# Optimization experiments

Measured on AMD Instinct MI355X. Metric: run time of the kernel, lower is better.

Reference implementation:

```python
import jax, jax.numpy as jnp
import numpy as np

H = 51      # hidden_size
IN = 1      # input_size
T = 512     # timesteps
B = 1024    # batch


def setup_inputs() -> dict:
    key = jax.random.key(0)
    ks = jax.random.split(key, 11)
    s = 1.0 / np.sqrt(H)  # PyTorch default init scale for LSTMCell/Linear
    u = lambda k, shape: jax.random.uniform(k, shape, jnp.float32, -s, s)
    return {
        "input": jax.random.normal(ks[0], (T, B, IN), jnp.float32),
        "W_ih1": u(ks[1], (4 * H, IN)),
        "W_hh1": u(ks[2], (4 * H, H)),
        "b_ih1": u(ks[3], (4 * H,)),
        "b_hh1": u(ks[4], (4 * H,)),
        "W_ih2": u(ks[5], (4 * H, H)),
        "W_hh2": u(ks[6], (4 * H, H)),
        "b_ih2": u(ks[7], (4 * H,)),
        "b_hh2": u(ks[8], (4 * H,)),
        "W_lin": u(ks[9], (1, H)),
        "b_lin": u(ks[10], (1,)),
        "future": 0,
    }


def _cell(x, h, c, W_ih, W_hh, b_ih, b_hh):
    # PyTorch LSTMCell: gates ordered (i, f, g, o)
    gates = x @ W_ih.T + h @ W_hh.T + (b_ih + b_hh)  # (B, 4H)
    i, f, g, o = jnp.split(gates, 4, axis=-1)
    c_new = jax.nn.sigmoid(f) * c + jax.nn.sigmoid(i) * jnp.tanh(g)
    h_new = jax.nn.sigmoid(o) * jnp.tanh(c_new)
    return h_new, c_new


def reference(input, W_ih1, W_hh1, b_ih1, b_hh1,
              W_ih2, W_hh2, b_ih2, b_hh2, W_lin, b_lin, future):
    n = input.shape[1]
    z = jnp.zeros((n, H), input.dtype)

    def step(carry, x_t):
        h1, c1, h2, c2 = carry
        h1, c1 = _cell(x_t, h1, c1, W_ih1, W_hh1, b_ih1, b_hh1)
        h2, c2 = _cell(h1, h2, c2, W_ih2, W_hh2, b_ih2, b_hh2)
        out = h2 @ W_lin.T + b_lin  # (B, 1)
        return (h1, c1, h2, c2), out

    carry, outs = jax.lax.scan(step, (z, z, z, z), input)  # outs: (T, B, 1)

    if future > 0:  # static Python int -> static branch
        def fstep(carry, _):
            h1, c1, h2, c2, out = carry
            h1, c1 = _cell(out, h1, c1, W_ih1, W_hh1, b_ih1, b_hh1)
            h2, c2 = _cell(h1, h2, c2, W_ih2, W_hh2, b_ih2, b_hh2)
            out = h2 @ W_lin.T + b_lin
            return (h1, c1, h2, c2, out), out

        h1, c1, h2, c2 = carry
        _, fouts = jax.lax.scan(fstep, (h1, c1, h2, c2, outs[-1]), None,
                                length=future)
        outs = jnp.concatenate([outs, fouts], axis=0)

    # torch cat(dim=1) of (B,1) slices -> (B, T+future)
    return outs[..., 0].T
```

## Files before the change

kernel.cpp:

```cpp
#include <hip/hip_runtime.h>


#define Hs    51
#define Ts    512
#define Bs    1024
#define NB    16
#define NT    512
#define SA    136
#define XCOL  51
#define H2COL 64

typedef __attribute__((ext_vector_type(8))) short bf16x8;
typedef __attribute__((ext_vector_type(4))) float f32x4;
typedef __attribute__((ext_vector_type(4))) int   i32x4;
typedef unsigned short u16;

__device__ __forceinline__ float sig_(float x)  { return 1.0f / (1.0f + __expf(-x)); }
__device__ __forceinline__ float tanh_(float x) { float e = __expf(2.0f * x); return 1.0f - 2.0f / (e + 1.0f); }
__device__ __forceinline__ u16 bfh_(float x) {
    unsigned u = __float_as_uint(x);
    return (u16)((u + 0x7FFFu + ((u >> 16) & 1u)) >> 16);
}
__device__ __forceinline__ float bff_(u16 h) { return __uint_as_float(((unsigned)h) << 16); }

struct FragHL { bf16x8 h; bf16x8 l; };

__device__ __forceinline__ FragHL mkB1(const float* __restrict__ Whh1,
                                       const float* __restrict__ Wih1,
                                       int row, bool rv, int ks, int ch) {
    bf16x8 h = {0,0,0,0,0,0,0,0}, l = {0,0,0,0,0,0,0,0};
    #pragma unroll
    for (int j = 0; j < 8; ++j) {
        const int k = ks * 32 + ch * 8 + j;
        float v = 0.f;
        if (rv) {
            if (k < Hs)         v = Whh1[row * Hs + k];
            else if (k == XCOL) v = Wih1[row];
        }
        u16 hh = bfh_(v);
        h[j] = (short)hh;
        l[j] = (short)bfh_(v - bff_(hh));
    }
    FragHL r; r.h = h; r.l = l; return r;
}

__device__ __forceinline__ FragHL mkB2(const float* __restrict__ Wih2,
                                       const float* __restrict__ Whh2,
                                       int row, bool rv, int ks, int ch) {
    bf16x8 h = {0,0,0,0,0,0,0,0}, l = {0,0,0,0,0,0,0,0};
    #pragma unroll
    for (int j = 0; j < 8; ++j) {
        const int k = ks * 32 + ch * 8 + j;
        float v = 0.f;
        if (rv) {
            if (k < Hs)                              v = Wih2[row * Hs + k];
            else if (k >= H2COL && k < H2COL + Hs)   v = Whh2[row * Hs + (k - H2COL)];
        }
        u16 hh = bfh_(v);
        h[j] = (short)hh;
        l[j] = (short)bfh_(v - bff_(hh));
    }
    FragHL r; r.h = h; r.l = l; return r;
}

__device__ __align__(16) u16   g_pack[NT * 32 * 8];
__device__ __align__(16) float g_bias[NT * 4];

__global__ __launch_bounds__(NT) void prep_kernel(
    const float* __restrict__ W_ih1, const float* __restrict__ W_hh1,
    const float* __restrict__ b_ih1, const float* __restrict__ b_hh1,
    const float* __restrict__ W_ih2, const float* __restrict__ W_hh2,
    const float* __restrict__ b_ih2, const float* __restrict__ b_hh2)
{
    const int tid  = threadIdx.x;
    const int lane = tid & 63;
    const int wv   = tid >> 6;
    const int role = wv >> 2;
    const int jg   = wv & 3;
    const int m    = lane & 15;
    const int ch   = lane >> 4;
    const int jrow = jg * 16 + m;
    const bool rv  = jrow < Hs;
    const int nks  = role ? 4 : 2;
    u16* base = &g_pack[tid * 256];

    for (int g = 0; g < 4; ++g) {
        const int row = g * Hs + jrow;
        g_bias[tid * 4 + g] = rv ? (role ? (b_ih2[row] + b_hh2[row])
                                         : (b_ih1[row] + b_hh1[row]))
                                 : 0.f;
        for (int s = 0; s < nks; ++s) {
            FragHL f = role ? mkB2(W_ih2, W_hh2, row, rv, s, ch)
                            : mkB1(W_hh1, W_ih1, row, rv, s, ch);
            *(bf16x8*)(base + (g * (2 * nks) + 2 * s + 0) * 8) = f.h;
            *(bf16x8*)(base + (g * (2 * nks) + 2 * s + 1) * 8) = f.l;
        }
    }
}

__device__ __forceinline__ bf16x8 ldfrag(const u16* p) {
    i32x4 v = *(const i32x4*)p;
    asm volatile("" : "+v"(v));
    union { i32x4 i; bf16x8 b; } u;
    u.i = v;
    return u.b;
}

#define MF(ACC, AFH, AFL, BH, BL)                                              \
    ACC = __builtin_amdgcn_mfma_f32_16x16x32_bf16(AFH, BL, ACC, 0, 0, 0);      \
    ACC = __builtin_amdgcn_mfma_f32_16x16x32_bf16(AFL, BH, ACC, 0, 0, 0);      \
    ACC = __builtin_amdgcn_mfma_f32_16x16x32_bf16(AFH, BH, ACC, 0, 0, 0);

__global__ __launch_bounds__(NT)
__attribute__((amdgpu_waves_per_eu(2, 2)))
void lstm2_kernel(
    const float* __restrict__ x,
    const float* __restrict__ W_lin,
    const float* __restrict__ b_lin,
    float* __restrict__ out)
{
    __shared__ __align__(16) u16   Ah[2][NB * SA];
    __shared__ __align__(16) u16   Al[2][NB * SA];
    __shared__ __align__(16) float xs[Ts][NB];
    __shared__ __align__(16) float h2f[2][NB][68];
    __shared__ __align__(16) float wlin_s[64];
    __shared__ float blin_sh;

    const int tid  = threadIdx.x;
    const int lane = tid & 63;
    const int wv   = tid >> 6;
    const int role = wv >> 2;
    const int jg   = wv & 3;
    const int m    = lane & 15;
    const int ch   = lane >> 4;
    const int bg0  = blockIdx.x * NB;
    const int  jrow = jg * 16 + m;
    const bool rv   = jrow < Hs;

    for (int i = tid; i < Ts * NB; i += NT) {
        int t = i >> 4, b = i & 15;
        xs[t][b] = x[t * Bs + bg0 + b];
    }
    for (int i = tid; i < 2 * NB * SA; i += NT) {
        ((u16*)Ah)[i] = 0;
        ((u16*)Al)[i] = 0;
    }
    for (int i = tid; i < 2 * NB * 68; i += NT) ((float*)h2f)[i] = 0.f;
    if (tid < 64) wlin_s[tid] = (tid < Hs) ? W_lin[tid] : 0.f;
    if (tid == 0) blin_sh = b_lin[0];
    __syncthreads();

    if (tid < NB) {
        float xv = x[bg0 + tid];
        u16 hh = bfh_(xv);
        Ah[1][tid * SA + XCOL] = hh;
        Al[1][tid * SA + XCOL] = bfh_(xv - bff_(hh));
    }

    f32x4 bb4 = *(const f32x4*)&g_bias[tid * 4];
    asm volatile("" : "+v"(bb4));
    const float bbI = bb4.x, bbF = bb4.y, bbG = bb4.z, bbO = bb4.w;

    const u16* pk = &g_pack[tid * 256];

    float cc0 = 0.f, cc1 = 0.f, cc2 = 0.f, cc3 = 0.f;
    __syncthreads();

    if (role == 0) {
        bf16x8 bI0h = ldfrag(pk + (0*4 + 0)*8), bI0l = ldfrag(pk + (0*4 + 1)*8);
        bf16x8 bI1h = ldfrag(pk + (0*4 + 2)*8), bI1l = ldfrag(pk + (0*4 + 3)*8);
        bf16x8 bF0h = ldfrag(pk + (1*4 + 0)*8), bF0l = ldfrag(pk + (1*4 + 1)*8);
        bf16x8 bF1h = ldfrag(pk + (1*4 + 2)*8), bF1l = ldfrag(pk + (1*4 + 3)*8);
        bf16x8 bG0h = ldfrag(pk + (2*4 + 0)*8), bG0l = ldfrag(pk + (2*4 + 1)*8);
        bf16x8 bG1h = ldfrag(pk + (2*4 + 2)*8), bG1l = ldfrag(pk + (2*4 + 3)*8);
        bf16x8 bO0h = ldfrag(pk + (3*4 + 0)*8), bO0l = ldfrag(pk + (3*4 + 1)*8);
        bf16x8 bO1h = ldfrag(pk + (3*4 + 2)*8), bO1l = ldfrag(pk + (3*4 + 3)*8);

        for (int it = 0; it <= Ts + 1; ++it) {
            const int pR = (it - 1) & 1;
            const int pW = it & 1;
            if (it < Ts) {
                const u16* ph = &Ah[pR][m * SA + ch * 8];
                const u16* pl = &Al[pR][m * SA + ch * 8];
                bf16x8 A0h = *(const bf16x8*)(ph);
                bf16x8 A0l = *(const bf16x8*)(pl);
                bf16x8 A1h = *(const bf16x8*)(ph + 32);
                bf16x8 A1l = *(const bf16x8*)(pl + 32);
                f32x4 aI = {bbI, bbI, bbI, bbI};
                f32x4 aF = {bbF, bbF, bbF, bbF};
                f32x4 aG = {bbG, bbG, bbG, bbG};
                f32x4 aO = {bbO, bbO, bbO, bbO};
                MF(aI, A0h, A0l, bI0h, bI0l)  MF(aF, A0h, A0l, bF0h, bF0l)
                MF(aG, A0h, A0l, bG0h, bG0l)  MF(aO, A0h, A0l, bO0h, bO0l)
                MF(aI, A1h, A1l, bI1h, bI1l)  MF(aF, A1h, A1l, bF1h, bF1l)
                MF(aG, A1h, A1l, bG1h, bG1l)  MF(aO, A1h, A1l, bO1h, bO1l)
                #define E1STEP(RR, CC)                                         \
                {                                                              \
                    float iv = sig_ (aI[RR]);                                  \
                    float fv = sig_ (aF[RR]);                                  \
                    float gv = tanh_(aG[RR]);                                  \
                    float ov = sig_ (aO[RR]);                                  \
                    CC = fmaf(fv, CC, iv * gv);                                \
                    float hv = ov * tanh_(CC);                                 \
                    if (rv) {                                                  \
                        const int b = 4 * ch + RR;                             \
                        u16 hh = bfh_(hv);                                     \
                        Ah[pW][b * SA + jrow] = hh;                            \
                        Al[pW][b * SA + jrow] = bfh_(hv - bff_(hh));           \
                    }                                                          \
                }
                E1STEP(0, cc0) E1STEP(1, cc1) E1STEP(2, cc2) E1STEP(3, cc3)
                #undef E1STEP
            }
            if (jg == 0 && lane < NB && (it + 1) < Ts) {
                float xv = xs[it + 1][lane];
                u16 hh = bfh_(xv);
                Ah[pW][lane * SA + XCOL] = hh;
                Al[pW][lane * SA + XCOL] = bfh_(xv - bff_(hh));
            }
            if (it >= 2) {
                const float* hp = &h2f[it & 1][4 * jg + ch][0];
                float s = wlin_s[m]      * hp[m]
                        + wlin_s[m + 16] * hp[m + 16]
                        + wlin_s[m + 32] * hp[m + 32]
                        + wlin_s[m + 48] * hp[m + 48];
                s += __shfl_xor(s, 1);
                s += __shfl_xor(s, 2);
                s += __shfl_xor(s, 4);
                s += __shfl_xor(s, 8);
                if (m == 0) out[(bg0 + 4 * jg + ch) * Ts + (it - 2)] = s + blin_sh;
            }
            __syncthreads();
        }
    } else {
        bf16x8 cI0h = ldfrag(pk + (0*8 + 0)*8), cI0l = ldfrag(pk + (0*8 + 1)*8);
        bf16x8 cI1h = ldfrag(pk + (0*8 + 2)*8), cI1l = ldfrag(pk + (0*8 + 3)*8);
        bf16x8 cI2h = ldfrag(pk + (0*8 + 4)*8), cI2l = ldfrag(pk + (0*8 + 5)*8);
        bf16x8 cI3h = ldfrag(pk + (0*8 + 6)*8), cI3l = ldfrag(pk + (0*8 + 7)*8);
        bf16x8 cF0h = ldfrag(pk + (1*8 + 0)*8), cF0l = ldfrag(pk + (1*8 + 1)*8);
        bf16x8 cF1h = ldfrag(pk + (1*8 + 2)*8), cF1l = ldfrag(pk + (1*8 + 3)*8);
        bf16x8 cF2h = ldfrag(pk + (1*8 + 4)*8), cF2l = ldfrag(pk + (1*8 + 5)*8);
        bf16x8 cF3h = ldfrag(pk + (1*8 + 6)*8), cF3l = ldfrag(pk + (1*8 + 7)*8);
        bf16x8 cG0h = ldfrag(pk + (2*8 + 0)*8), cG0l = ldfrag(pk + (2*8 + 1)*8);
        bf16x8 cG1h = ldfrag(pk + (2*8 + 2)*8), cG1l = ldfrag(pk + (2*8 + 3)*8);
        bf16x8 cG2h = ldfrag(pk + (2*8 + 4)*8), cG2l = ldfrag(pk + (2*8 + 5)*8);
        bf16x8 cG3h = ldfrag(pk + (2*8 + 6)*8), cG3l = ldfrag(pk + (2*8 + 7)*8);
        bf16x8 cO0h = ldfrag(pk + (3*8 + 0)*8), cO0l = ldfrag(pk + (3*8 + 1)*8);
        bf16x8 cO1h = ldfrag(pk + (3*8 + 2)*8), cO1l = ldfrag(pk + (3*8 + 3)*8);
        bf16x8 cO2h = ldfrag(pk + (3*8 + 4)*8), cO2l = ldfrag(pk + (3*8 + 5)*8);
        bf16x8 cO3h = ldfrag(pk + (3*8 + 6)*8), cO3l = ldfrag(pk + (3*8 + 7)*8);

        for (int it = 0; it <= Ts + 1; ++it) {
            const int pR = (it - 1) & 1;
            const int pW = it & 1;
            if (it >= 1 && it <= Ts) {
                const u16* ph = &Ah[pR][m * SA + ch * 8];
                const u16* pl = &Al[pR][m * SA + ch * 8];
                bf16x8 A0h = *(const bf16x8*)(ph);
                bf16x8 A0l = *(const bf16x8*)(pl);
                bf16x8 A1h = *(const bf16x8*)(ph + 32);
                bf16x8 A1l = *(const bf16x8*)(pl + 32);
                bf16x8 A2h = *(const bf16x8*)(ph + 64);
                bf16x8 A2l = *(const bf16x8*)(pl + 64);
                bf16x8 A3h = *(const bf16x8*)(ph + 96);
                bf16x8 A3l = *(const bf16x8*)(pl + 96);
                f32x4 aI = {bbI, bbI, bbI, bbI};
                f32x4 aF = {bbF, bbF, bbF, bbF};
                f32x4 aG = {bbG, bbG, bbG, bbG};
                f32x4 aO = {bbO, bbO, bbO, bbO};
                MF(aI, A0h, A0l, cI0h, cI0l)  MF(aF, A0h, A0l, cF0h, cF0l)
                MF(aG, A0h, A0l, cG0h, cG0l)  MF(aO, A0h, A0l, cO0h, cO0l)
                MF(aI, A1h, A1l, cI1h, cI1l)  MF(aF, A1h, A1l, cF1h, cF1l)
                MF(aG, A1h, A1l, cG1h, cG1l)  MF(aO, A1h, A1l, cO1h, cO1l)
                MF(aI, A2h, A2l, cI2h, cI2l)  MF(aF, A2h, A2l, cF2h, cF2l)
                MF(aG, A2h, A2l, cG2h, cG2l)  MF(aO, A2h, A2l, cO2h, cO2l)
                MF(aI, A3h, A3l, cI3h, cI3l)  MF(aF, A3h, A3l, cF3h, cF3l)
                MF(aG, A3h, A3l, cG3h, cG3l)  MF(aO, A3h, A3l, cO3h, cO3l)
                const int pE = (it - 1) & 1;
                #define E2STEP(RR, CC)                                         \
                {                                                              \
                    float iv = sig_ (aI[RR]);                                  \
                    float fv = sig_ (aF[RR]);                                  \
                    float gv = tanh_(aG[RR]);                                  \
                    float ov = sig_ (aO[RR]);                                  \
                    CC = fmaf(fv, CC, iv * gv);                                \
                    float hv = ov * tanh_(CC);                                 \
                    if (rv) {                                                  \
                        const int b = 4 * ch + RR;                             \
                        u16 hh = bfh_(hv);                                     \
                        Ah[pW][b * SA + H2COL + jrow] = hh;                    \
                        Al[pW][b * SA + H2COL + jrow] = bfh_(hv - bff_(hh));   \
                        h2f[pE][b][jrow] = hv;                                 \
                    }                                                          \
                }
                E2STEP(0, cc0) E2STEP(1, cc1) E2STEP(2, cc2) E2STEP(3, cc3)
                #undef E2STEP
            }
            __syncthreads();
        }
    }
}

extern "C" void kernel_launch(void* const* d_in, const int* in_sizes, int n_in,
                              void* d_out, int out_size, void* d_ws, size_t ws_size,
                              hipStream_t stream) {
    const float* x     = (const float*)d_in[0];
    const float* W_ih1 = (const float*)d_in[1];
    const float* W_hh1 = (const float*)d_in[2];
    const float* b_ih1 = (const float*)d_in[3];
    const float* b_hh1 = (const float*)d_in[4];
    const float* W_ih2 = (const float*)d_in[5];
    const float* W_hh2 = (const float*)d_in[6];
    const float* b_ih2 = (const float*)d_in[7];
    const float* b_hh2 = (const float*)d_in[8];
    const float* W_lin = (const float*)d_in[9];
    const float* b_lin = (const float*)d_in[10];
    float* out = (float*)d_out;

    prep_kernel<<<1, NT, 0, stream>>>(W_ih1, W_hh1, b_ih1, b_hh1,
                                      W_ih2, W_hh2, b_ih2, b_hh2);
    lstm2_kernel<<<Bs / NB, NT, 0, stream>>>(x, W_lin, b_lin, out);
}
```

Baseline: 1.052 ms.

## Split MFMA accumulation chains, precompute split-bf16 inputs, buffer outputs in LDS

Each gate's hi/lo bf16 MFMA products now go into independent accumulator chains that are summed at the end, replacing one long dependent chain, to cut MFMA latency on the recurrent critical path. Input x is split into hi/lo bf16 once during preload rather than every step. Linear-layer outputs are collected in a shared-memory buffer and written to global memory coalesced after the loop, instead of as strided per-step stores. The waves_per_eu attribute is dropped and W_lin is hoisted into registers, which may raise register pressure and change occupancy; the extra 32KB of LDS also counts against the shared-memory budget.

```diff
diff --git a/kernel.cpp b/kernel.cpp
--- a/kernel.cpp
+++ b/kernel.cpp
@@ -106,24 +106,21 @@
     return u.b;
 }
 
-#define MF(ACC, AFH, AFL, BH, BL)                                              \
-    ACC = __builtin_amdgcn_mfma_f32_16x16x32_bf16(AFH, BL, ACC, 0, 0, 0);      \
-    ACC = __builtin_amdgcn_mfma_f32_16x16x32_bf16(AFL, BH, ACC, 0, 0, 0);      \
-    ACC = __builtin_amdgcn_mfma_f32_16x16x32_bf16(AFH, BH, ACC, 0, 0, 0);
+#define MFMA_(A, B, C) __builtin_amdgcn_mfma_f32_16x16x32_bf16(A, B, C, 0, 0, 0)
 
 __global__ __launch_bounds__(NT)
-__attribute__((amdgpu_waves_per_eu(2, 2)))
 void lstm2_kernel(
     const float* __restrict__ x,
     const float* __restrict__ W_lin,
     const float* __restrict__ b_lin,
     float* __restrict__ out)
 {
-    __shared__ __align__(16) u16   Ah[2][NB * SA];
-    __shared__ __align__(16) u16   Al[2][NB * SA];
-    __shared__ __align__(16) float xs[Ts][NB];
-    __shared__ __align__(16) float h2f[2][NB][68];
-    __shared__ __align__(16) float wlin_s[64];
+    __shared__ __align__(16) u16      Ah[2][NB * SA];
+    __shared__ __align__(16) u16      Al[2][NB * SA];
+    __shared__ __align__(16) unsigned xs32[Ts][NB];
+    __shared__ __align__(16) float    h2f[2][NB][68];
+    __shared__ __align__(16) float    ybuf[NB][Ts];
+    __shared__ __align__(16) float    wlin_s[64];
     __shared__ float blin_sh;
 
     const int tid  = threadIdx.x;
@@ -139,7 +136,10 @@
 
     for (int i = tid; i < Ts * NB; i += NT) {
         int t = i >> 4, b = i & 15;
-        xs[t][b] = x[t * Bs + bg0 + b];
+        float xv = x[t * Bs + bg0 + b];
+        u16 hh = bfh_(xv);
+        u16 hl = bfh_(xv - bff_(hh));
+        xs32[t][b] = (unsigned)hh | ((unsigned)hl << 16);
     }
     for (int i = tid; i < 2 * NB * SA; i += NT) {
         ((u16*)Ah)[i] = 0;
@@ -151,10 +151,9 @@
     __syncthreads();
 
     if (tid < NB) {
-        float xv = x[bg0 + tid];
-        u16 hh = bfh_(xv);
-        Ah[1][tid * SA + XCOL] = hh;
-        Al[1][tid * SA + XCOL] = bfh_(xv - bff_(hh));
+        unsigned v = xs32[0][tid];
+        Ah[1][tid * SA + XCOL] = (u16)v;
+        Al[1][tid * SA + XCOL] = (u16)(v >> 16);
     }
 
     f32x4 bb4 = *(const f32x4*)&g_bias[tid * 4];
@@ -165,6 +164,10 @@
 
     float cc0 = 0.f, cc1 = 0.f, cc2 = 0.f, cc3 = 0.f;
     __syncthreads();
+
+    const float wl0 = wlin_s[m],      wl1 = wlin_s[m + 16];
+    const float wl2 = wlin_s[m + 32], wl3 = wlin_s[m + 48];
+    const float blin_r = blin_sh;
 
     if (role == 0) {
         bf16x8 bI0h = ldfrag(pk + (0*4 + 0)*8), bI0l = ldfrag(pk + (0*4 + 1)*8);
@@ -186,14 +189,22 @@
                 bf16x8 A0l = *(const bf16x8*)(pl);
                 bf16x8 A1h = *(const bf16x8*)(ph + 32);
                 bf16x8 A1l = *(const bf16x8*)(pl + 32);
-                f32x4 aI = {bbI, bbI, bbI, bbI};
-                f32x4 aF = {bbF, bbF, bbF, bbF};
-                f32x4 aG = {bbG, bbG, bbG, bbG};
-                f32x4 aO = {bbO, bbO, bbO, bbO};
-                MF(aI, A0h, A0l, bI0h, bI0l)  MF(aF, A0h, A0l, bF0h, bF0l)
-                MF(aG, A0h, A0l, bG0h, bG0l)  MF(aO, A0h, A0l, bO0h, bO0l)
-                MF(aI, A1h, A1l, bI1h, bI1l)  MF(aF, A1h, A1l, bF1h, bF1l)
-                MF(aG, A1h, A1l, bG1h, bG1l)  MF(aO, A1h, A1l, bO1h, bO1l)
+                #define L1GATE(OUT, BB, B0h, B0l, B1h, B1l)                    \
+                {                                                              \
+                    f32x4 p = {BB, BB, BB, BB};                                \
+                    f32x4 q = {0.f, 0.f, 0.f, 0.f};                            \
+                    f32x4 r = {0.f, 0.f, 0.f, 0.f};                            \
+                    p = MFMA_(A0h, B0h, p); p = MFMA_(A1h, B1h, p);            \
+                    q = MFMA_(A0l, B0h, q); q = MFMA_(A1l, B1h, q);            \
+                    r = MFMA_(A0h, B0l, r); r = MFMA_(A1h, B1l, r);            \
+                    OUT = (p + q) + r;                                         \
+                }
+                f32x4 aI, aF, aG, aO;
+                L1GATE(aI, bbI, bI0h, bI0l, bI1h, bI1l)
+                L1GATE(aF, bbF, bF0h, bF0l, bF1h, bF1l)
+                L1GATE(aG, bbG, bG0h, bG0l, bG1h, bG1l)
+                L1GATE(aO, bbO, bO0h, bO0l, bO1h, bO1l)
+                #undef L1GATE
                 #define E1STEP(RR, CC)                                         \
                 {                                                              \
                     float iv = sig_ (aI[RR]);                                  \
@@ -213,22 +224,19 @@
                 #undef E1STEP
             }
             if (jg == 0 && lane < NB && (it + 1) < Ts) {
-                float xv = xs[it + 1][lane];
-                u16 hh = bfh_(xv);
-                Ah[pW][lane * SA + XCOL] = hh;
-                Al[pW][lane * SA + XCOL] = bfh_(xv - bff_(hh));
+                unsigned v = xs32[it + 1][lane];
+                Ah[pW][lane * SA + XCOL] = (u16)v;
+                Al[pW][lane * SA + XCOL] = (u16)(v >> 16);
             }
             if (it >= 2) {
                 const float* hp = &h2f[it & 1][4 * jg + ch][0];
-                float s = wlin_s[m]      * hp[m]
-                        + wlin_s[m + 16] * hp[m + 16]
-                        + wlin_s[m + 32] * hp[m + 32]
-                        + wlin_s[m + 48] * hp[m + 48];
+                float s = wl0 * hp[m] + wl1 * hp[m + 16]
+                        + wl2 * hp[m + 32] + wl3 * hp[m + 48];
                 s += __shfl_xor(s, 1);
                 s += __shfl_xor(s, 2);
                 s += __shfl_xor(s, 4);
                 s += __shfl_xor(s, 8);
-                if (m == 0) out[(bg0 + 4 * jg + ch) * Ts + (it - 2)] = s + blin_sh;
+                if (m == 0) ybuf[4 * jg + ch][it - 2] = s + blin_r;
             }
             __syncthreads();
         }
@@ -264,18 +272,24 @@
                 bf16x8 A2l = *(const bf16x8*)(pl + 64);
                 bf16x8 A3h = *(const bf16x8*)(ph + 96);
                 bf16x8 A3l = *(const bf16x8*)(pl + 96);
-                f32x4 aI = {bbI, bbI, bbI, bbI};
-                f32x4 aF = {bbF, bbF, bbF, bbF};
-                f32x4 aG = {bbG, bbG, bbG, bbG};
-                f32x4 aO = {bbO, bbO, bbO, bbO};
-                MF(aI, A0h, A0l, cI0h, cI0l)  MF(aF, A0h, A0l, cF0h, cF0l)
-                MF(aG, A0h, A0l, cG0h, cG0l)  MF(aO, A0h, A0l, cO0h, cO0l)
-                MF(aI, A1h, A1l, cI1h, cI1l)  MF(aF, A1h, A1l, cF1h, cF1l)
-                MF(aG, A1h, A1l, cG1h, cG1l)  MF(aO, A1h, A1l, cO1h, cO1l)
-                MF(aI, A2h, A2l, cI2h, cI2l)  MF(aF, A2h, A2l, cF2h, cF2l)
-                MF(aG, A2h, A2l, cG2h, cG2l)  MF(aO, A2h, A2l, cO2h, cO2l)
-                MF(aI, A3h, A3l, cI3h, cI3l)  MF(aF, A3h, A3l, cF3h, cF3l)
-                MF(aG, A3h, A3l, cG3h, cG3l)  MF(aO, A3h, A3l, cO3h, cO3l)
+                #define L2GATE(OUT, BB, C0h, C0l, C1h, C1l, C2h, C2l, C3h, C3l)\
+                {                                                              \
+                    f32x4 p = {BB, BB, BB, BB};                                \
+                    f32x4 r = {0.f, 0.f, 0.f, 0.f};                            \
+                    p = MFMA_(A0h, C0h, p); p = MFMA_(A1h, C1h, p);            \
+                    p = MFMA_(A2h, C2h, p); p = MFMA_(A3h, C3h, p);            \
+                    p = MFMA_(A0l, C0h, p); p = MFMA_(A1l, C1h, p);            \
+                    p = MFMA_(A2l, C2h, p); p = MFMA_(A3l, C3h, p);            \
+                    r = MFMA_(A0h, C0l, r); r = MFMA_(A1h, C1l, r);            \
+                    r = MFMA_(A2h, C2l, r); r = MFMA_(A3h, C3l, r);            \
+                    OUT = p + r;                                               \
+                }
+                f32x4 aI, aF, aG, aO;
+                L2GATE(aI, bbI, cI0h, cI0l, cI1h, cI1l, cI2h, cI2l, cI3h, cI3l)
+                L2GATE(aF, bbF, cF0h, cF0l, cF1h, cF1l, cF2h, cF2l, cF3h, cF3l)
+                L2GATE(aG, bbG, cG0h, cG0l, cG1h, cG1l, cG2h, cG2l, cG3h, cG3l)
+                L2GATE(aO, bbO, cO0h, cO0l, cO1h, cO1l, cO2h, cO2l, cO3h, cO3l)
+                #undef L2GATE
                 const int pE = (it - 1) & 1;
                 #define E2STEP(RR, CC)                                         \
                 {                                                              \
@@ -299,6 +313,12 @@
             __syncthreads();
         }
     }
+
+    __syncthreads();
+    for (int i = tid; i < NB * Ts; i += NT) {
+        int b = i >> 9, t = i & (Ts - 1);
+        out[(bg0 + b) * Ts + t] = ybuf[b][t];
+    }
 }
 
 extern "C" void kernel_launch(void* const* d_in, const int* in_sizes, int n_in,
```

After: 1.114 ms. +5.9%, slower.

## Merge layer-1 and layer-2 wave roles into single 256-thread block per batch tile

Applied to the files above, without the earlier changes.

Instead of 8 waves split into layer-1 and layer-2 roles, each of 4 waves now computes both LSTM layers sequentially within a timestep, holding both weight sets in registers. Block size halves and waves-per-EU is set to 1, cutting barrier participants and letting each wave run more work per barrier. The input is also pre-split into bf16 hi/lo pairs once at load time, and the linear-head weights are hoisted into registers. The cost is serialising the two layers' MFMA chains within a wave (less parallelism per step) and much higher register pressure.

```diff
diff --git a/kernel.cpp b/kernel.cpp
--- a/kernel.cpp
+++ b/kernel.cpp
@@ -5,7 +5,7 @@
 #define Ts    512
 #define Bs    1024
 #define NB    16
-#define NT    512
+#define NT    256
 #define SA    136
 #define XCOL  51
 #define H2COL 64
@@ -63,8 +63,8 @@
     FragHL r; r.h = h; r.l = l; return r;
 }
 
-__device__ __align__(16) u16   g_pack[NT * 32 * 8];
-__device__ __align__(16) float g_bias[NT * 4];
+__device__ __align__(16) u16   g_pack[NT * 48 * 8];
+__device__ __align__(16) float g_bias[NT * 8];
 
 __global__ __launch_bounds__(NT) void prep_kernel(
     const float* __restrict__ W_ih1, const float* __restrict__ W_hh1,
@@ -74,26 +74,26 @@
 {
     const int tid  = threadIdx.x;
     const int lane = tid & 63;
-    const int wv   = tid >> 6;
-    const int role = wv >> 2;
-    const int jg   = wv & 3;
+    const int jg   = tid >> 6;
     const int m    = lane & 15;
     const int ch   = lane >> 4;
     const int jrow = jg * 16 + m;
     const bool rv  = jrow < Hs;
-    const int nks  = role ? 4 : 2;
-    u16* base = &g_pack[tid * 256];
+    u16* base = &g_pack[tid * 384];
 
     for (int g = 0; g < 4; ++g) {
         const int row = g * Hs + jrow;
-        g_bias[tid * 4 + g] = rv ? (role ? (b_ih2[row] + b_hh2[row])
-                                         : (b_ih1[row] + b_hh1[row]))
-                                 : 0.f;
-        for (int s = 0; s < nks; ++s) {
-            FragHL f = role ? mkB2(W_ih2, W_hh2, row, rv, s, ch)
-                            : mkB1(W_hh1, W_ih1, row, rv, s, ch);
-            *(bf16x8*)(base + (g * (2 * nks) + 2 * s + 0) * 8) = f.h;
-            *(bf16x8*)(base + (g * (2 * nks) + 2 * s + 1) * 8) = f.l;
+        g_bias[tid * 8 + g]     = rv ? (b_ih1[row] + b_hh1[row]) : 0.f;
+        g_bias[tid * 8 + 4 + g] = rv ? (b_ih2[row] + b_hh2[row]) : 0.f;
+        for (int s = 0; s < 2; ++s) {
+            FragHL f = mkB1(W_hh1, W_ih1, row, rv, s, ch);
+            *(bf16x8*)(base + (g * 4 + s * 2 + 0) * 8) = f.h;
+            *(bf16x8*)(base + (g * 4 + s * 2 + 1) * 8) = f.l;
+        }
+        for (int s = 0; s < 4; ++s) {
+            FragHL f = mkB2(W_ih2, W_hh2, row, rv, s, ch);
+            *(bf16x8*)(base + (16 + g * 8 + s * 2 + 0) * 8) = f.h;
+            *(bf16x8*)(base + (16 + g * 8 + s * 2 + 1) * 8) = f.l;
         }
     }
 }
@@ -106,31 +106,30 @@
     return u.b;
 }
 
+#define MFMA_(A, B, C) __builtin_amdgcn_mfma_f32_16x16x32_bf16(A, B, C, 0, 0, 0)
 #define MF(ACC, AFH, AFL, BH, BL)                                              \
-    ACC = __builtin_amdgcn_mfma_f32_16x16x32_bf16(AFH, BL, ACC, 0, 0, 0);      \
-    ACC = __builtin_amdgcn_mfma_f32_16x16x32_bf16(AFL, BH, ACC, 0, 0, 0);      \
-    ACC = __builtin_amdgcn_mfma_f32_16x16x32_bf16(AFH, BH, ACC, 0, 0, 0);
+    ACC = MFMA_(AFH, BL, ACC);                                                 \
+    ACC = MFMA_(AFL, BH, ACC);                                                 \
+    ACC = MFMA_(AFH, BH, ACC);
 
 __global__ __launch_bounds__(NT)
-__attribute__((amdgpu_waves_per_eu(2, 2)))
+__attribute__((amdgpu_waves_per_eu(1, 1)))
 void lstm2_kernel(
     const float* __restrict__ x,
     const float* __restrict__ W_lin,
     const float* __restrict__ b_lin,
     float* __restrict__ out)
 {
-    __shared__ __align__(16) u16   Ah[2][NB * SA];
-    __shared__ __align__(16) u16   Al[2][NB * SA];
-    __shared__ __align__(16) float xs[Ts][NB];
-    __shared__ __align__(16) float h2f[2][NB][68];
-    __shared__ __align__(16) float wlin_s[64];
+    __shared__ __align__(16) u16      Ah[2][NB * SA];
+    __shared__ __align__(16) u16      Al[2][NB * SA];
+    __shared__ __align__(16) unsigned xs32[Ts][NB];
+    __shared__ __align__(16) float    h2f[2][NB][68];
+    __shared__ __align__(16) float    wlin_s[64];
     __shared__ float blin_sh;
 
     const int tid  = threadIdx.x;
     const int lane = tid & 63;
-    const int wv   = tid >> 6;
-    const int role = wv >> 2;
-    const int jg   = wv & 3;
+    const int jg   = tid >> 6;
     const int m    = lane & 15;
     const int ch   = lane >> 4;
     const int bg0  = blockIdx.x * NB;
@@ -139,7 +138,10 @@
 
     for (int i = tid; i < Ts * NB; i += NT) {
         int t = i >> 4, b = i & 15;
-        xs[t][b] = x[t * Bs + bg0 + b];
+        float xv = x[t * Bs + bg0 + b];
+        u16 hh = bfh_(xv);
+        u16 hl = bfh_(xv - bff_(hh));
+        xs32[t][b] = (unsigned)hh | ((unsigned)hl << 16);
     }
     for (int i = tid; i < 2 * NB * SA; i += NT) {
         ((u16*)Ah)[i] = 0;
@@ -151,153 +153,151 @@
     __syncthreads();
 
     if (tid < NB) {
-        float xv = x[bg0 + tid];
-        u16 hh = bfh_(xv);
-        Ah[1][tid * SA + XCOL] = hh;
-        Al[1][tid * SA + XCOL] = bfh_(xv - bff_(hh));
-    }
-
-    f32x4 bb4 = *(const f32x4*)&g_bias[tid * 4];
-    asm volatile("" : "+v"(bb4));
-    const float bbI = bb4.x, bbF = bb4.y, bbG = bb4.z, bbO = bb4.w;
-
-    const u16* pk = &g_pack[tid * 256];
-
-    float cc0 = 0.f, cc1 = 0.f, cc2 = 0.f, cc3 = 0.f;
+        unsigned v = xs32[0][tid];
+        Ah[1][tid * SA + XCOL] = (u16)v;
+        Al[1][tid * SA + XCOL] = (u16)(v >> 16);
+    }
+
+    f32x4 bb1 = *(const f32x4*)&g_bias[tid * 8];
+    f32x4 bb2 = *(const f32x4*)&g_bias[tid * 8 + 4];
+    asm volatile("" : "+v"(bb1));
+    asm volatile("" : "+v"(bb2));
+    const float b1I = bb1.x, b1F = bb1.y, b1G = bb1.z, b1O = bb1.w;
+    const float b2I = bb2.x, b2F = bb2.y, b2G = bb2.z, b2O = bb2.w;
+
+    const u16* pk = &g_pack[tid * 384];
+
+    bf16x8 bI0h = ldfrag(pk + (0*4+0)*8), bI0l = ldfrag(pk + (0*4+1)*8);
+    bf16x8 bI1h = ldfrag(pk + (0*4+2)*8), bI1l = ldfrag(pk + (0*4+3)*8);
+    bf16x8 bF0h = ldfrag(pk + (1*4+0)*8), bF0l = ldfrag(pk + (1*4+1)*8);
+    bf16x8 bF1h = ldfrag(pk + (1*4+2)*8), bF1l = ldfrag(pk + (1*4+3)*8);
+    bf16x8 bG0h = ldfrag(pk + (2*4+0)*8), bG0l = ldfrag(pk + (2*4+1)*8);
+    bf16x8 bG1h = ldfrag(pk + (2*4+2)*8), bG1l = ldfrag(pk + (2*4+3)*8);
+    bf16x8 bO0h = ldfrag(pk + (3*4+0)*8), bO0l = ldfrag(pk + (3*4+1)*8);
+    bf16x8 bO1h = ldfrag(pk + (3*4+2)*8), bO1l = ldfrag(pk + (3*4+3)*8);
+    bf16x8 cI0h = ldfrag(pk + (16+0*8+0)*8), cI0l = ldfrag(pk + (16+0*8+1)*8);
+    bf16x8 cI1h = ldfrag(pk + (16+0*8+2)*8), cI1l = ldfrag(pk + (16+0*8+3)*8);
+    bf16x8 cI2h = ldfrag(pk + (16+0*8+4)*8), cI2l = ldfrag(pk + (16+0*8+5)*8);
+    bf16x8 cI3h = ldfrag(pk + (16+0*8+6)*8), cI3l = ldfrag(pk + (16+0*8+7)*8);
+    bf16x8 cF0h = ldfrag(pk + (16+1*8+0)*8), cF0l = ldfrag(pk + (16+1*8+1)*8);
+    bf16x8 cF1h = ldfrag(pk + (16+1*8+2)*8), cF1l = ldfrag(pk + (16+1*8+3)*8);
+    bf16x8 cF2h = ldfrag(pk + (16+1*8+4)*8), cF2l = ldfrag(pk + (16+1*8+5)*8);
+    bf16x8 cF3h = ldfrag(pk + (16+1*8+6)*8), cF3l = ldfrag(pk + (16+1*8+7)*8);
+    bf16x8 cG0h = ldfrag(pk + (16+2*8+0)*8), cG0l = ldfrag(pk + (16+2*8+1)*8);
+    bf16x8 cG1h = ldfrag(pk + (16+2*8+2)*8), cG1l = ldfrag(pk + (16+2*8+3)*8);
+    bf16x8 cG2h = ldfrag(pk + (16+2*8+4)*8), cG2l = ldfrag(pk + (16+2*8+5)*8);
+    bf16x8 cG3h = ldfrag(pk + (16+2*8+6)*8), cG3l = ldfrag(pk + (16+2*8+7)*8);
+    bf16x8 cO0h = ldfrag(pk + (16+3*8+0)*8), cO0l = ldfrag(pk + (16+3*8+1)*8);
+    bf16x8 cO1h = ldfrag(pk + (16+3*8+2)*8), cO1l = ldfrag(pk + (16+3*8+3)*8);
+    bf16x8 cO2h = ldfrag(pk + (16+3*8+4)*8), cO2l = ldfrag(pk + (16+3*8+5)*8);
+    bf16x8 cO3h = ldfrag(pk + (16+3*8+6)*8), cO3l = ldfrag(pk + (16+3*8+7)*8);
+
+    float c10 = 0.f, c11 = 0.f, c12 = 0.f, c13 = 0.f;
+    float c20 = 0.f, c21 = 0.f, c22 = 0.f, c23 = 0.f;
     __syncthreads();
 
-    if (role == 0) {
-        bf16x8 bI0h = ldfrag(pk + (0*4 + 0)*8), bI0l = ldfrag(pk + (0*4 + 1)*8);
-        bf16x8 bI1h = ldfrag(pk + (0*4 + 2)*8), bI1l = ldfrag(pk + (0*4 + 3)*8);
-        bf16x8 bF0h = ldfrag(pk + (1*4 + 0)*8), bF0l = ldfrag(pk + (1*4 + 1)*8);
-        bf16x8 bF1h = ldfrag(pk + (1*4 + 2)*8), bF1l = ldfrag(pk + (1*4 + 3)*8);
-        bf16x8 bG0h = ldfrag(pk + (2*4 + 0)*8), bG0l = ldfrag(pk + (2*4 + 1)*8);
-        bf16x8 bG1h = ldfrag(pk + (2*4 + 2)*8), bG1l = ldfrag(pk + (2*4 + 3)*8);
-        bf16x8 bO0h = ldfrag(pk + (3*4 + 0)*8), bO0l = ldfrag(pk + (3*4 + 1)*8);
-        bf16x8 bO1h = ldfrag(pk + (3*4 + 2)*8), bO1l = ldfrag(pk + (3*4 + 3)*8);
-
-        for (int it = 0; it <= Ts + 1; ++it) {
-            const int pR = (it - 1) & 1;
-            const int pW = it & 1;
-            if (it < Ts) {
-                const u16* ph = &Ah[pR][m * SA + ch * 8];
-                const u16* pl = &Al[pR][m * SA + ch * 8];
-                bf16x8 A0h = *(const bf16x8*)(ph);
-                bf16x8 A0l = *(const bf16x8*)(pl);
-                bf16x8 A1h = *(const bf16x8*)(ph + 32);
-                bf16x8 A1l = *(const bf16x8*)(pl + 32);
-                f32x4 aI = {bbI, bbI, bbI, bbI};
-                f32x4 aF = {bbF, bbF, bbF, bbF};
-                f32x4 aG = {bbG, bbG, bbG, bbG};
-                f32x4 aO = {bbO, bbO, bbO, bbO};
-                MF(aI, A0h, A0l, bI0h, bI0l)  MF(aF, A0h, A0l, bF0h, bF0l)
-                MF(aG, A0h, A0l, bG0h, bG0l)  MF(aO, A0h, A0l, bO0h, bO0l)
-                MF(aI, A1h, A1l, bI1h, bI1l)  MF(aF, A1h, A1l, bF1h, bF1l)
-                MF(aG, A1h, A1l, bG1h, bG1l)  MF(aO, A1h, A1l, bO1h, bO1l)
-                #define E1STEP(RR, CC)                                         \
-                {                                                              \
-                    float iv = sig_ (aI[RR]);                                  \
-                    float fv = sig_ (aF[RR]);                                  \
-                    float gv = tanh_(aG[RR]);                                  \
-                    float ov = sig_ (aO[RR]);                                  \
-                    CC = fmaf(fv, CC, iv * gv);                                \
-                    float hv = ov * tanh_(CC);                                 \
-                    if (rv) {                                                  \
-                        const int b = 4 * ch + RR;                             \
-                        u16 hh = bfh_(hv);                                     \
-                        Ah[pW][b * SA + jrow] = hh;                            \
-                        Al[pW][b * SA + jrow] = bfh_(hv - bff_(hh));           \
-                    }                                                          \
-                }
-                E1STEP(0, cc0) E1STEP(1, cc1) E1STEP(2, cc2) E1STEP(3, cc3)
-                #undef E1STEP
+    const float wl0 = wlin_s[m],      wl1 = wlin_s[m + 16];
+    const float wl2 = wlin_s[m + 32], wl3 = wlin_s[m + 48];
+    const float blin_r = blin_sh;
+
+    for (int it = 0; it <= Ts + 1; ++it) {
+        const int pR = (it - 1) & 1;
+        const int pW = it & 1;
+
+        if (it < Ts) {
+            const u16* ph = &Ah[pR][m * SA + ch * 8];
+            const u16* pl = &Al[pR][m * SA + ch * 8];
+            bf16x8 A0h = *(const bf16x8*)(ph);
+            bf16x8 A0l = *(const bf16x8*)(pl);
+            bf16x8 A1h = *(const bf16x8*)(ph + 32);
+            bf16x8 A1l = *(const bf16x8*)(pl + 32);
+            f32x4 aI = {b1I, b1I, b1I, b1I};
+            f32x4 aF = {b1F, b1F, b1F, b1F};
+            f32x4 aG = {b1G, b1G, b1G, b1G};
+            f32x4 aO = {b1O, b1O, b1O, b1O};
+            MF(aI, A0h, A0l, bI0h, bI0l)  MF(aF, A0h, A0l, bF0h, bF0l)
+            MF(aG, A0h, A0l, bG0h, bG0l)  MF(aO, A0h, A0l, bO0h, bO0l)
+            MF(aI, A1h, A1l, bI1h, bI1l)  MF(aF, A1h, A1l, bF1h, bF1l)
+            MF(aG, A1h, A1l, bG1h, bG1l)  MF(aO, A1h, A1l, bO1h, bO1l)
+            #define E1STEP(RR, CC)                                             \
+            {                                                                  \
+                float iv = sig_ (aI[RR]);                                      \
+                float fv = sig_ (aF[RR]);                                      \
+                float gv = tanh_(aG[RR]);                                      \
+                float ov = sig_ (aO[RR]);                                      \
+                CC = fmaf(fv, CC, iv * gv);                                    \
+                float hv = ov * tanh_(CC);                                     \
+                if (rv) {                                                      \
+                    const int b = 4 * ch + RR;                                 \
+                    u16 hh = bfh_(hv);                                         \
+                    Ah[pW][b * SA + jrow] = hh;                                \
+                    Al[pW][b * SA + jrow] = bfh_(hv - bff_(hh));               \
+                }                                                              \
             }
-            if (jg == 0 && lane < NB && (it + 1) < Ts) {
-                float xv = xs[it + 1][lane];
-                u16 hh = bfh_(xv);
-                Ah[pW][lane * SA + XCOL] = hh;
-                Al[pW][lane * SA + XCOL] = bfh_(xv - bff_(hh));
+            E1STEP(0, c10) E1STEP(1, c11) E1STEP(2, c12) E1STEP(3, c13)
+            #undef E1STEP
+        }
+
+        if (it >= 1 && it <= Ts) {
+            const u16* ph = &Ah[pR][m * SA + ch * 8];
+            const u16* pl = &Al[pR][m * SA + ch * 8];
+            bf16x8 A0h = *(const bf16x8*)(ph);
+            bf16x8 A0l = *(const bf16x8*)(pl);
+            bf16x8 A1h = *(const bf16x8*)(ph + 32);
+            bf16x8 A1l = *(const bf16x8*)(pl + 32);
+            bf16x8 A2h = *(const bf16x8*)(ph + 64);
+            bf16x8 A2l = *(const bf16x8*)(pl + 64);
+            bf16x8 A3h = *(const bf16x8*)(ph + 96);
+            bf16x8 A3l = *(const bf16x8*)(pl + 96);
+            f32x4 aI = {b2I, b2I, b2I, b2I};
+            f32x4 aF = {b2F, b2F, b2F, b2F};
+            f32x4 aG = {b2G, b2G, b2G, b2G};
+            f32x4 aO = {b2O, b2O, b2O, b2O};
+            MF(aI, A0h, A0l, cI0h, cI0l)  MF(aF, A0h, A0l, cF0h, cF0l)
+            MF(aG, A0h, A0l, cG0h, cG0l)  MF(aO, A0h, A0l, cO0h, cO0l)
+            MF(aI, A1h, A1l, cI1h, cI1l)  MF(aF, A1h, A1l, cF1h, cF1l)
+            MF(aG, A1h, A1l, cG1h, cG1l)  MF(aO, A1h, A1l, cO1h, cO1l)
+            MF(aI, A2h, A2l, cI2h, cI2l)  MF(aF, A2h, A2l, cF2h, cF2l)
+            MF(aG, A2h, A2l, cG2h, cG2l)  MF(aO, A2h, A2l, cO2h, cO2l)
+            MF(aI, A3h, A3l, cI3h, cI3l)  MF(aF, A3h, A3l, cF3h, cF3l)
+            MF(aG, A3h, A3l, cG3h, cG3l)  MF(aO, A3h, A3l, cO3h, cO3l)
+            const int pE = (it - 1) & 1;
+            #define E2STEP(RR, CC)                                             \
+            {                                                                  \
+                float iv = sig_ (aI[RR]);                                      \
+                float fv = sig_ (aF[RR]);                                      \
+                float gv = tanh_(aG[RR]);                                      \
+                float ov = sig_ (aO[RR]);                                      \
+                CC = fmaf(fv, CC, iv * gv);                                    \
+                float hv = ov * tanh_(CC);                                     \
+                if (rv) {                                                      \
+                    const int b = 4 * ch + RR;                                 \
+                    u16 hh = bfh_(hv);                                         \
+                    Ah[pW][b * SA + H2COL + jrow] = hh;                        \
+                    Al[pW][b * SA + H2COL + jrow] = bfh_(hv - bff_(hh));       \
+                    h2f[pE][b][jrow] = hv;                                     \
+                }                                                              \
             }
-            if (it >= 2) {
-                const float* hp = &h2f[it & 1][4 * jg + ch][0];
-                float s = wlin_s[m]      * hp[m]
-                        + wlin_s[m + 16] * hp[m + 16]
-                        + wlin_s[m + 32] * hp[m + 32]
-                        + wlin_s[m + 48] * hp[m + 48];
-                s += __shfl_xor(s, 1);
-                s += __shfl_xor(s, 2);
-                s += __shfl_xor(s, 4);
-                s += __shfl_xor(s, 8);
-                if (m == 0) out[(bg0 + 4 * jg + ch) * Ts + (it - 2)] = s + blin_sh;
-            }
-            __syncthreads();
-        }
-    } else {
-        bf16x8 cI0h = ldfrag(pk + (0*8 + 0)*8), cI0l = ldfrag(pk + (0*8 + 1)*8);
-        bf16x8 cI1h = ldfrag(pk + (0*8 + 2)*8), cI1l = ldfrag(pk + (0*8 + 3)*8);
-        bf16x8 cI2h = ldfrag(pk + (0*8 + 4)*8), cI2l = ldfrag(pk + (0*8 + 5)*8);
-        bf16x8 cI3h = ldfrag(pk + (0*8 + 6)*8), cI3l = ldfrag(pk + (0*8 + 7)*8);
-        bf16x8 cF0h = ldfrag(pk + (1*8 + 0)*8), cF0l = ldfrag(pk + (1*8 + 1)*8);
-        bf16x8 cF1h = ldfrag(pk + (1*8 + 2)*8), cF1l = ldfrag(pk + (1*8 + 3)*8);
-        bf16x8 cF2h = ldfrag(pk + (1*8 + 4)*8), cF2l = ldfrag(pk + (1*8 + 5)*8);
-        bf16x8 cF3h = ldfrag(pk + (1*8 + 6)*8), cF3l = ldfrag(pk + (1*8 + 7)*8);
-        bf16x8 cG0h = ldfrag(pk + (2*8 + 0)*8), cG0l = ldfrag(pk + (2*8 + 1)*8);
-        bf16x8 cG1h = ldfrag(pk + (2*8 + 2)*8), cG1l = ldfrag(pk + (2*8 + 3)*8);
-        bf16x8 cG2h = ldfrag(pk + (2*8 + 4)*8), cG2l = ldfrag(pk + (2*8 + 5)*8);
-        bf16x8 cG3h = ldfrag(pk + (2*8 + 6)*8), cG3l = ldfrag(pk + (2*8 + 7)*8);
-        bf16x8 cO0h = ldfrag(pk + (3*8 + 0)*8), cO0l = ldfrag(pk + (3*8 + 1)*8);
-        bf16x8 cO1h = ldfrag(pk + (3*8 + 2)*8), cO1l = ldfrag(pk + (3*8 + 3)*8);
-        bf16x8 cO2h = ldfrag(pk + (3*8 + 4)*8), cO2l = ldfrag(pk + (3*8 + 5)*8);
-        bf16x8 cO3h = ldfrag(pk + (3*8 + 6)*8), cO3l = ldfrag(pk + (3*8 + 7)*8);
-
-        for (int it = 0; it <= Ts + 1; ++it) {
-            const int pR = (it - 1) & 1;
-            const int pW = it & 1;
-            if (it >= 1 && it <= Ts) {
-                const u16* ph = &Ah[pR][m * SA + ch * 8];
-                const u16* pl = &Al[pR][m * SA + ch * 8];
-                bf16x8 A0h = *(const bf16x8*)(ph);
-                bf16x8 A0l = *(const bf16x8*)(pl);
-                bf16x8 A1h = *(const bf16x8*)(ph + 32);
-                bf16x8 A1l = *(const bf16x8*)(pl + 32);
-                bf16x8 A2h = *(const bf16x8*)(ph + 64);
-                bf16x8 A2l = *(const bf16x8*)(pl + 64);
-                bf16x8 A3h = *(const bf16x8*)(ph + 96);
-                bf16x8 A3l = *(const bf16x8*)(pl + 96);
-                f32x4 aI = {bbI, bbI, bbI, bbI};
-                f32x4 aF = {bbF, bbF, bbF, bbF};
-                f32x4 aG = {bbG, bbG, bbG, bbG};
-                f32x4 aO = {bbO, bbO, bbO, bbO};
-                MF(aI, A0h, A0l, cI0h, cI0l)  MF(aF, A0h, A0l, cF0h, cF0l)
-                MF(aG, A0h, A0l, cG0h, cG0l)  MF(aO, A0h, A0l, cO0h, cO0l)
-                MF(aI, A1h, A1l, cI1h, cI1l)  MF(aF, A1h, A1l, cF1h, cF1l)
-                MF(aG, A1h, A1l, cG1h, cG1l)  MF(aO, A1h, A1l, cO1h, cO1l)
-                MF(aI, A2h, A2l, cI2h, cI2l)  MF(aF, A2h, A2l, cF2h, cF2l)
-                MF(aG, A2h, A2l, cG2h, cG2l)  MF(aO, A2h, A2l, cO2h, cO2l)
-                MF(aI, A3h, A3l, cI3h, cI3l)  MF(aF, A3h, A3l, cF3h, cF3l)
-                MF(aG, A3h, A3l, cG3h, cG3l)  MF(aO, A3h, A3l, cO3h, cO3l)
-                const int pE = (it - 1) & 1;
-                #define E2STEP(RR, CC)                                         \
-                {                                                              \
-                    float iv = sig_ (aI[RR]);                                  \
-                    float fv = sig_ (aF[RR]);                                  \
-                    float gv = tanh_(aG[RR]);                                  \
-                    float ov = sig_ (aO[RR]);                                  \
-                    CC = fmaf(fv, CC, iv * gv);                                \
-                    float hv = ov * tanh_(CC);                                 \
-                    if (rv) {                                                  \
-                        const int b = 4 * ch + RR;                             \
-                        u16 hh = bfh_(hv);                                     \
-                        Ah[pW][b * SA + H2COL + jrow] = hh;                    \
-                        Al[pW][b * SA + H2COL + jrow] = bfh_(hv - bff_(hh));   \
-                        h2f[pE][b][jrow] = hv;                                 \
-                    }                                                          \
-                }
-                E2STEP(0, cc0) E2STEP(1, cc1) E2STEP(2, cc2) E2STEP(3, cc3)
-                #undef E2STEP
-            }
-            __syncthreads();
-        }
+            E2STEP(0, c20) E2STEP(1, c21) E2STEP(2, c22) E2STEP(3, c23)
+            #undef E2STEP
+        }
+
+        if (jg == 0 && lane < NB && (it + 1) < Ts) {
+            unsigned v = xs32[it + 1][lane];
+            Ah[pW][lane * SA + XCOL] = (u16)v;
+            Al[pW][lane * SA + XCOL] = (u16)(v >> 16);
+        }
+        if (it >= 2) {
+            const float* hp = &h2f[it & 1][4 * jg + ch][0];
+            float s = wl0 * hp[m] + wl1 * hp[m + 16]
+                    + wl2 * hp[m + 32] + wl3 * hp[m + 48];
+            s += __shfl_xor(s, 1);
+            s += __shfl_xor(s, 2);
+            s += __shfl_xor(s, 4);
+            s += __shfl_xor(s, 8);
+            if (m == 0) out[(bg0 + 4 * jg + ch) * Ts + (it - 2)] = s + blin_r;
+        }
+        __syncthreads();
     }
 }
 
```

Result: slower. 1.408 ms (+33.9%).
